# Optimization experiments

Hardware: AMD Instinct MI355X
Metric: run time of the kernel (lower is better)

The kernel has to match this reference:

```python
import jax, jax.numpy as jnp
import numpy as np

N = 100000       # nodes
E = 1600000      # edges
F_IN = 128       # num_node_features
H = 256          # graph_hidden_channels
NHID = 512
NOUT = 256
G = 256          # graphs in batch


def setup_inputs() -> dict:
    key = jax.random.key(0)
    ks = jax.random.split(key, 14)
    x = jax.random.normal(ks[0], (N, F_IN), jnp.float32)
    src = jax.random.randint(ks[1], (E,), 0, N, jnp.int32)
    dst = jax.random.randint(ks[2], (E,), 0, N, jnp.int32)
    batch = jnp.sort(jax.random.randint(ks[3], (N,), 0, G, jnp.int32))
    def lin(k, fan_in, fan_out):
        return jax.random.normal(k, (fan_in, fan_out), jnp.float32) * (1.0 / np.sqrt(fan_in))
    return {
        "x": x, "src": src, "dst": dst, "batch": batch,
        "W1": lin(ks[4], F_IN, H), "b1": jnp.zeros((H,), jnp.float32),
        "W2": lin(ks[5], H, H),    "b2": jnp.zeros((H,), jnp.float32),
        "W3": lin(ks[6], H, H),    "b3": jnp.zeros((H,), jnp.float32),
        "Wm1": lin(ks[7], H, NHID), "bm1": jnp.zeros((NHID,), jnp.float32),
        "Wm2": lin(ks[8], NHID, NOUT), "bm2": jnp.zeros((NOUT,), jnp.float32),
    }


def _gcn_layer(h_in, W, b, src, dst, dinv):
    # GCNConv: transform, then symmetric-normalized aggregation with self-loops.
    h = h_in @ W                                            # [N, out]
    norm = (dinv[src] * dinv[dst])[:, None]                 # [E, 1]
    agg = jax.ops.segment_sum(h[src] * norm, dst, num_segments=N)
    agg = agg + h * (dinv * dinv)[:, None]                  # self-loop term (norm = 1/deg)
    return agg + b


def reference(x, src, dst, batch, W1, b1, W2, b2, W3, b3, Wm1, bm1, Wm2, bm2):
    # degrees include the added self-loop (+1)
    deg = 1.0 + jax.ops.segment_sum(jnp.ones((E,), x.dtype), dst, num_segments=N)
    dinv = jax.lax.rsqrt(deg)                               # deg^{-1/2}

    h = jax.nn.relu(_gcn_layer(x, W1, b1, src, dst, dinv))
    h = jax.nn.relu(_gcn_layer(h, W2, b2, src, dst, dinv))
    h = _gcn_layer(h, W3, b3, src, dst, dinv)               # no relu before pooling

    # global mean pool over graphs
    counts = jax.ops.segment_sum(jnp.ones((N,), x.dtype), batch, num_segments=G)
    pooled = jax.ops.segment_sum(h, batch, num_segments=G) / jnp.maximum(counts, 1.0)[:, None]

    out = jax.nn.relu(pooled @ Wm1 + bm1) @ Wm2 + bm2       # [G, NOUT]
    return out
```

## Files before the change

### kernel.cpp

```cpp
#include <hip/hip_runtime.h>
#include <hip/hip_bf16.h>

#define N_NODES 100000
#define N_EDGES 1600000
#define F_IN    128
#define H       256
#define NHID    512
#define NOUT    256
#define G_GR    256

typedef unsigned short u16;
typedef __attribute__((ext_vector_type(8))) short s16x8;
typedef __attribute__((ext_vector_type(8))) unsigned short u16x8;
typedef __attribute__((ext_vector_type(4))) float f32x4;

__device__ __forceinline__ float bf2f(u16 u) {
    union { unsigned int i; float f; } v; v.i = ((unsigned int)u) << 16; return v.f;
}
__device__ __forceinline__ u16 f2bf(float f) {
    union { float f; unsigned int i; } v; v.f = f;
    unsigned int x = v.i;
    x += 0x7fffu + ((x >> 16) & 1u);
    return (u16)(x >> 16);
}

#define CD_BLKS   1563
#define SPX_BLKS  ((N_NODES * F_IN) / 1024)
#define T1_BLKS   ((F_IN * H) / 256)
#define T2_BLKS   ((H * H) / 256)
#define T3_BLKS   ((H * H) / 256)
#define TM1_BLKS  ((H * NHID) / 256)
#define TM2_BLKS  ((NHID * NOUT) / 256)
#define HEAD_BLKS (CD_BLKS + T1_BLKS + T2_BLKS + T3_BLKS + TM1_BLKS + TM2_BLKS + 2)

__device__ __forceinline__ void transpose_split_body(const float* __restrict__ W,
        u16* __restrict__ thi, u16* __restrict__ tlo, int K, int N, int id) {
    int n = id / K, k = id - n * K;
    float f = W[(size_t)k * N + n];
    u16 h = f2bf(f);
    thi[id] = h;
    tlo[id] = f2bf(f - bf2f(h));
}

__global__ __launch_bounds__(256) void prep_head(
        const int* __restrict__ dst, int* __restrict__ degc,
        const float* __restrict__ W1, u16* __restrict__ t1h, u16* __restrict__ t1l,
        const float* __restrict__ W2, u16* __restrict__ t2h, u16* __restrict__ t2l,
        const float* __restrict__ W3, u16* __restrict__ t3h, u16* __restrict__ t3l,
        const float* __restrict__ Wm1, u16* __restrict__ tm1h, u16* __restrict__ tm1l,
        const float* __restrict__ Wm2, u16* __restrict__ tm2h, u16* __restrict__ tm2l,
        const int* __restrict__ batch, int* __restrict__ goff) {
    int bid = blockIdx.x;
    if (bid < CD_BLKS) {
        int base = bid * 1024 + threadIdx.x;
#pragma unroll
        for (int q = 0; q < 4; q++) {
            int e = base + q * 256;
            if (e < N_EDGES) atomicAdd(&degc[dst[e]], 1);
        }
        return;
    }
    bid -= CD_BLKS;
    if (bid < T1_BLKS) {
        transpose_split_body(W1, t1h, t1l, F_IN, H, bid * 256 + threadIdx.x);
        return;
    }
    bid -= T1_BLKS;
    if (bid < T2_BLKS) {
        transpose_split_body(W2, t2h, t2l, H, H, bid * 256 + threadIdx.x);
        return;
    }
    bid -= T2_BLKS;
    if (bid < T3_BLKS) {
        transpose_split_body(W3, t3h, t3l, H, H, bid * 256 + threadIdx.x);
        return;
    }
    bid -= T3_BLKS;
    if (bid < TM1_BLKS) {
        transpose_split_body(Wm1, tm1h, tm1l, H, NHID, bid * 256 + threadIdx.x);
        return;
    }
    bid -= TM1_BLKS;
    if (bid < TM2_BLKS) {
        transpose_split_body(Wm2, tm2h, tm2l, NHID, NOUT, bid * 256 + threadIdx.x);
        return;
    }
    bid -= TM2_BLKS;
    {
        int g = bid * 256 + threadIdx.x;
        if (g > G_GR) return;
        int lo = 0, hi = N_NODES;
        while (lo < hi) {
            int mid = (lo + hi) >> 1;
            if (batch[mid] < g) lo = mid + 1; else hi = mid;
        }
        goff[g] = lo;
    }
}

__global__ void scan_partial(const int* __restrict__ cnt, int* __restrict__ partial) {
    __shared__ int s[256];
    int t = threadIdx.x;
    int i = blockIdx.x * 256 + t;
    int v = (i < N_NODES) ? cnt[i] : 0;
    s[t] = v; __syncthreads();
    for (int off = 128; off > 0; off >>= 1) {
        if (t < off) s[t] += s[t + off];
        __syncthreads();
    }
    if (t == 0) partial[blockIdx.x] = s[0];
}

__global__ void scan_offsets(int* __restrict__ partial, int nb, int* __restrict__ rowp) {
    __shared__ int s[512];
    int t = threadIdx.x;
    int orig = (t < nb) ? partial[t] : 0;
    s[t] = orig; __syncthreads();
    for (int off = 1; off < 512; off <<= 1) {
        int u = (t >= off) ? s[t - off] : 0;
        __syncthreads();
        s[t] += u;
        __syncthreads();
    }
    if (t < nb) partial[t] = s[t] - orig;
    if (t == 0) rowp[N_NODES] = N_EDGES;
}

__global__ void scan_final_dinv(const int* __restrict__ cnt, const int* __restrict__ partial,
                                int* __restrict__ rowp, int* __restrict__ cur,
                                float* __restrict__ dinv) {
    __shared__ int s[256];
    int t = threadIdx.x;
    int i = blockIdx.x * 256 + t;
    int v = (i < N_NODES) ? cnt[i] : 0;
    s[t] = v; __syncthreads();
    for (int off = 1; off < 256; off <<= 1) {
        int u = (t >= off) ? s[t - off] : 0;
        __syncthreads();
        s[t] += u;
        __syncthreads();
    }
    if (i < N_NODES) {
        int r = partial[blockIdx.x] + s[t] - v;
        rowp[i] = r;
        cur[i] = r;
        dinv[i] = rsqrtf(1.0f + (float)v);
    }
}

__global__ __launch_bounds__(256) void scatter_splitx(
        const int* __restrict__ src, const int* __restrict__ dst,
        const float* __restrict__ dinv, int* __restrict__ cur,
        int2* __restrict__ ep,
        const float* __restrict__ x, u16* __restrict__ x_bf) {
    int bid = blockIdx.x;
    if (bid < CD_BLKS) {
        int base = bid * 1024 + threadIdx.x;
#pragma unroll
        for (int q = 0; q < 4; q++) {
            int e = base + q * 256;
            if (e < N_EDGES) {
                int d = dst[e];
                int s = src[e];
                float w = dinv[d] * dinv[s];
                int pos = atomicAdd(&cur[d], 1);
                int2 v; v.x = s; v.y = __float_as_int(w);
                ep[pos] = v;
            }
        }
        return;
    }
    bid -= CD_BLKS;
    {
        int idx = bid * 256 + threadIdx.x;
        float4 f = *(const float4*)&x[(size_t)idx * 4];
        ushort4 o;
        o.x = f2bf(f.x); o.y = f2bf(f.y); o.z = f2bf(f.z); o.w = f2bf(f.w);
        *(ushort4*)&x_bf[(size_t)idx * 4] = o;
    }
}

__global__ __launch_bounds__(256) void gcn_agg256(
        const u16* __restrict__ in, const int* __restrict__ rowp,
        const int2* __restrict__ ep, const float* __restrict__ dinv,
        u16* __restrict__ outp) {
    int node = blockIdx.x * 8 + (threadIdx.x >> 5);
    int l = threadIdx.x & 31;
    int beg = rowp[node], end = rowp[node + 1];
    float a[8] = {};
    int e = beg;
    int2 pr[8];
    bool have = (e + 8 <= end);
    if (have) {
#pragma unroll
        for (int q = 0; q < 8; q++) pr[q] = ep[e + q];
    }
    while (have) {
        int2 g8[8];
#pragma unroll
        for (int q = 0; q < 8; q++) g8[q] = pr[q];
        int en = e + 8;
        bool haven = (en + 8 <= end);
        if (haven) {
#pragma unroll
            for (int q = 0; q < 8; q++) pr[q] = ep[en + q];
        }
#pragma unroll
        for (int q = 0; q < 8; q++) {
            u16x8 u = *(const u16x8*)&in[(size_t)g8[q].x * H + l * 8];
            float wt = __int_as_float(g8[q].y);
#pragma unroll
            for (int r = 0; r < 8; r++) a[r] += bf2f(u[r]) * wt;
        }
        e = en; have = haven;
    }
    for (; e < end; e++) {
        int2 pe = ep[e];
        float wt = __int_as_float(pe.y);
        u16x8 u = *(const u16x8*)&in[(size_t)pe.x * H + l * 8];
#pragma unroll
        for (int r = 0; r < 8; r++) a[r] += bf2f(u[r]) * wt;
    }
    float di = dinv[node];
    u16x8 us = *(const u16x8*)&in[(size_t)node * H + l * 8];
    float dd = di * di;
    u16x8 o;
#pragma unroll
    for (int r = 0; r < 8; r++) o[r] = f2bf(a[r] + bf2f(us[r]) * dd);
    *(u16x8*)&outp[(size_t)node * H + l * 8] = o;
}

__global__ __launch_bounds__(256) void gcn_agg128(
        const u16* __restrict__ in, const int* __restrict__ rowp,
        const int2* __restrict__ ep, const float* __restrict__ dinv,
        u16* __restrict__ outp) {
    int node = blockIdx.x * 16 + (threadIdx.x >> 4);
    int l = threadIdx.x & 15;
    int beg = rowp[node], end = rowp[node + 1];
    float a[8] = {};
    int e = beg;
    int2 pr[8];
    bool have = (e + 8 <= end);
    if (have) {
#pragma unroll
        for (int q = 0; q < 8; q++) pr[q] = ep[e + q];
    }
    while (have) {
        int2 g8[8];
#pragma unroll
        for (int q = 0; q < 8; q++) g8[q] = pr[q];
        int en = e + 8;
        bool haven = (en + 8 <= end);
        if (haven) {
#pragma unroll
            for (int q = 0; q < 8; q++) pr[q] = ep[en + q];
        }
#pragma unroll
        for (int q = 0; q < 8; q++) {
            u16x8 u = *(const u16x8*)&in[(size_t)g8[q].x * F_IN + l * 8];
            float wt = __int_as_float(g8[q].y);
#pragma unroll
            for (int r = 0; r < 8; r++) a[r] += bf2f(u[r]) * wt;
        }
        e = en; have = haven;
    }
    for (; e < end; e++) {
        int2 pe = ep[e];
        float wt = __int_as_float(pe.y);
        u16x8 u = *(const u16x8*)&in[(size_t)pe.x * F_IN + l * 8];
#pragma unroll
        for (int r = 0; r < 8; r++) a[r] += bf2f(u[r]) * wt;
    }
    float di = dinv[node];
    u16x8 us = *(const u16x8*)&in[(size_t)node * F_IN + l * 8];
    float dd = di * di;
    u16x8 o;
#pragma unroll
    for (int r = 0; r < 8; r++) o[r] = f2bf(a[r] + bf2f(us[r]) * dd);
    *(u16x8*)&outp[(size_t)node * F_IN + l * 8] = o;
}

__global__ __launch_bounds__(256) void gcn_agg_pool(
        const u16* __restrict__ in, const int* __restrict__ rowp,
        const int2* __restrict__ ep, const float* __restrict__ dinv,
        const int* __restrict__ batch, float* __restrict__ poolacc) {
    __shared__ __align__(16) float pacc[8][H];
    __shared__ int gslot[8];
    const int tid = threadIdx.x;
    const int hw = tid >> 5;
    const int l = tid & 31;
    const int node = blockIdx.x * 8 + hw;
    const int gbase = batch[blockIdx.x * 8];

    int beg = rowp[node], end = rowp[node + 1];
    float a[8] = {};
    int e = beg;
    int2 pr[8];
    bool have = (e + 8 <= end);
    if (have) {
#pragma unroll
        for (int q = 0; q < 8; q++) pr[q] = ep[e + q];
    }
    while (have) {
        int2 g8[8];
#pragma unroll
        for (int q = 0; q < 8; q++) g8[q] = pr[q];
        int en = e + 8;
        bool haven = (en + 8 <= end);
        if (haven) {
#pragma unroll
            for (int q = 0; q < 8; q++) pr[q] = ep[en + q];
        }
#pragma unroll
        for (int q = 0; q < 8; q++) {
            u16x8 u = *(const u16x8*)&in[(size_t)g8[q].x * H + l * 8];
            float wt = __int_as_float(g8[q].y);
#pragma unroll
            for (int r = 0; r < 8; r++) a[r] += bf2f(u[r]) * wt;
        }
        e = en; have = haven;
    }
    for (; e < end; e++) {
        int2 pe = ep[e];
        float wt = __int_as_float(pe.y);
        u16x8 u = *(const u16x8*)&in[(size_t)pe.x * H + l * 8];
#pragma unroll
        for (int r = 0; r < 8; r++) a[r] += bf2f(u[r]) * wt;
    }
    float di = dinv[node];
    u16x8 us = *(const u16x8*)&in[(size_t)node * H + l * 8];
    float dd = di * di;
    f32x4 lo4, hi4;
#pragma unroll
    for (int r = 0; r < 4; r++) lo4[r] = a[r] + bf2f(us[r]) * dd;
#pragma unroll
    for (int r = 0; r < 4; r++) hi4[r] = a[r + 4] + bf2f(us[r + 4]) * dd;
    *(f32x4*)&pacc[hw][l * 8] = lo4;
    *(f32x4*)&pacc[hw][l * 8 + 4] = hi4;
    if (l == 0) gslot[hw] = batch[node] - gbase;
    __syncthreads();

    int smax = gslot[7];
    float v[8];
#pragma unroll
    for (int q = 0; q < 8; q++) v[q] = pacc[q][tid];
    for (int s = 0; s <= smax; s++) {
        float acc = 0.f;
#pragma unroll
        for (int q = 0; q < 8; q++)
            if (gslot[q] == s) acc += v[q];
        atomicAdd(&poolacc[(size_t)(gbase + s) * H + tid], acc);
    }
}

__global__ __launch_bounds__(256) void pool_finalize2(
        const float* __restrict__ poolacc, const int* __restrict__ goff,
        u16* __restrict__ phi, u16* __restrict__ plo) {
    int g = blockIdx.x, t = threadIdx.x;
    float c = (float)(goff[g + 1] - goff[g]);
    float acc = poolacc[(size_t)g * H + t] / fmaxf(c, 1.f);
    u16 hv = f2bf(acc);
    phi[g * H + t] = hv;
    plo[g * H + t] = f2bf(acc - bf2f(hv));
}

template<int K, bool RELU>
__global__ __launch_bounds__(256) void gemm_bias(
        const u16* __restrict__ A,
        const u16* __restrict__ Bhi, const u16* __restrict__ Blo,
        const float* __restrict__ bias, u16* __restrict__ C, int M) {
    __shared__ __align__(16) u16 sA[128 * 40];
    __shared__ __align__(16) u16 sB[2 * 128 * 40];
    const int tid = threadIdx.x;
    const int w = tid >> 6, l = tid & 63;
    const int wm = (w & 1) * 64, wn = (w >> 1) * 64;
    const int bm = blockIdx.x * 128, bn = blockIdx.y * 128;
    const int srow = tid >> 2;
    const int schunk = (tid & 3) * 8;
    const int lr = l & 15, lg = (l >> 4) * 8;

    f32x4 acc[4][4] = {};

    for (int k0 = 0; k0 < K; k0 += 32) {
        {
            int r0 = bm + srow, r1 = bm + srow + 64;
            u16x8 v0 = {}, v1 = {};
            if (r0 < M) v0 = *(const u16x8*)&A[(size_t)r0 * K + k0 + schunk];
            if (r1 < M) v1 = *(const u16x8*)&A[(size_t)r1 * K + k0 + schunk];
            *(u16x8*)&sA[srow * 40 + schunk] = v0;
            *(u16x8*)&sA[(srow + 64) * 40 + schunk] = v1;
        }
        {
            int n0 = bn + srow, n1 = bn + srow + 64;
            *(u16x8*)&sB[srow * 40 + schunk] = *(const u16x8*)&Bhi[(size_t)n0 * K + k0 + schunk];
            *(u16x8*)&sB[(srow + 64) * 40 + schunk] = *(const u16x8*)&Bhi[(size_t)n1 * K + k0 + schunk];
            *(u16x8*)&sB[128 * 40 + srow * 40 + schunk] = *(const u16x8*)&Blo[(size_t)n0 * K + k0 + schunk];
            *(u16x8*)&sB[128 * 40 + (srow + 64) * 40 + schunk] = *(const u16x8*)&Blo[(size_t)n1 * K + k0 + schunk];
        }
        __syncthreads();

        s16x8 af[4], bh[4], bl[4];
#pragma unroll
        for (int i = 0; i < 4; i++)
            af[i] = __builtin_bit_cast(s16x8, *(const u16x8*)&sA[(wm + i * 16 + lr) * 40 + lg]);
#pragma unroll
        for (int j = 0; j < 4; j++) {
            bh[j] = __builtin_bit_cast(s16x8, *(const u16x8*)&sB[(wn + j * 16 + lr) * 40 + lg]);
            bl[j] = __builtin_bit_cast(s16x8, *(const u16x8*)&sB[128 * 40 + (wn + j * 16 + lr) * 40 + lg]);
        }
#pragma unroll
        for (int i = 0; i < 4; i++) {
#pragma unroll
            for (int j = 0; j < 4; j++) {
                acc[i][j] = __builtin_amdgcn_mfma_f32_16x16x32_bf16(af[i], bh[j], acc[i][j], 0, 0, 0);
                acc[i][j] = __builtin_amdgcn_mfma_f32_16x16x32_bf16(af[i], bl[j], acc[i][j], 0, 0, 0);
            }
        }
        __syncthreads();
    }

    float bcol[4];
#pragma unroll
    for (int j = 0; j < 4; j++) bcol[j] = bias[bn + wn + j * 16 + lr];

    const int lq = (l >> 4) * 4;
#pragma unroll
    for (int i = 0; i < 4; i++) {
#pragma unroll
        for (int r0 = 0; r0 < 4; r0++) {
            int row = bm + wm + i * 16 + lq + r0;
            if (row < M) {
#pragma unroll
                for (int j = 0; j < 4; j++) {
                    float v = acc[i][j][r0] + bcol[j];
                    if (RELU) v = fmaxf(v, 0.f);
                    C[(size_t)row * H + bn + wn + j * 16 + lr] = f2bf(v);
                }
            }
        }
    }
}

template<int K, int NW, bool RELU, bool F32OUT>
__global__ __launch_bounds__(256) void gemm_split(
        const u16* __restrict__ Ahi, const u16* __restrict__ Alo,
        const u16* __restrict__ Bhi, const u16* __restrict__ Blo,
        const float* __restrict__ bias,
        u16* __restrict__ Chi, u16* __restrict__ Clo, float* __restrict__ Cf,
        int M) {
    __shared__ __align__(16) u16 sA[2 * 128 * 40];
    __shared__ __align__(16) u16 sB[2 * 128 * 40];
    const int tid = threadIdx.x;
    const int w = tid >> 6, l = tid & 63;
    const int wm = (w & 1) * 64, wn = (w >> 1) * 64;
    const int bm = blockIdx.x * 128, bn = blockIdx.y * 128;
    const int srow = tid >> 2;
    const int schunk = (tid & 3) * 8;
    const int lr = l & 15, lg = (l >> 4) * 8;

    f32x4 acc[4][4] = {};

    for (int k0 = 0; k0 < K; k0 += 32) {
        {
            int r0 = bm + srow, r1 = bm + srow + 64;
            u16x8 v0 = {}, v1 = {}, w0 = {}, w1 = {};
            if (r0 < M) {
                v0 = *(const u16x8*)&Ahi[(size_t)r0 * K + k0 + schunk];
                w0 = *(const u16x8*)&Alo[(size_t)r0 * K + k0 + schunk];
            }
            if (r1 < M) {
                v1 = *(const u16x8*)&Ahi[(size_t)r1 * K + k0 + schunk];
                w1 = *(const u16x8*)&Alo[(size_t)r1 * K + k0 + schunk];
            }
            *(u16x8*)&sA[srow * 40 + schunk] = v0;
            *(u16x8*)&sA[(srow + 64) * 40 + schunk] = v1;
            *(u16x8*)&sA[128 * 40 + srow * 40 + schunk] = w0;
            *(u16x8*)&sA[128 * 40 + (srow + 64) * 40 + schunk] = w1;
        }
        {
            int n0 = bn + srow, n1 = bn + srow + 64;
            *(u16x8*)&sB[srow * 40 + schunk] = *(const u16x8*)&Bhi[(size_t)n0 * K + k0 + schunk];
            *(u16x8*)&sB[(srow + 64) * 40 + schunk] = *(const u16x8*)&Bhi[(size_t)n1 * K + k0 + schunk];
            *(u16x8*)&sB[128 * 40 + srow * 40 + schunk] = *(const u16x8*)&Blo[(size_t)n0 * K + k0 + schunk];
            *(u16x8*)&sB[128 * 40 + (srow + 64) * 40 + schunk] = *(const u16x8*)&Blo[(size_t)n1 * K + k0 + schunk];
        }
        __syncthreads();

        s16x8 af[4], al[4], bh[4], bl[4];
#pragma unroll
        for (int i = 0; i < 4; i++) {
            af[i] = __builtin_bit_cast(s16x8, *(const u16x8*)&sA[(wm + i * 16 + lr) * 40 + lg]);
            al[i] = __builtin_bit_cast(s16x8, *(const u16x8*)&sA[128 * 40 + (wm + i * 16 + lr) * 40 + lg]);
        }
#pragma unroll
        for (int j = 0; j < 4; j++) {
            bh[j] = __builtin_bit_cast(s16x8, *(const u16x8*)&sB[(wn + j * 16 + lr) * 40 + lg]);
            bl[j] = __builtin_bit_cast(s16x8, *(const u16x8*)&sB[128 * 40 + (wn + j * 16 + lr) * 40 + lg]);
        }
#pragma unroll
        for (int i = 0; i < 4; i++) {
#pragma unroll
            for (int j = 0; j < 4; j++) {
                acc[i][j] = __builtin_amdgcn_mfma_f32_16x16x32_bf16(af[i], bh[j], acc[i][j], 0, 0, 0);
                acc[i][j] = __builtin_amdgcn_mfma_f32_16x16x32_bf16(af[i], bl[j], acc[i][j], 0, 0, 0);
                acc[i][j] = __builtin_amdgcn_mfma_f32_16x16x32_bf16(al[i], bh[j], acc[i][j], 0, 0, 0);
            }
        }
        __syncthreads();
    }

    float bcol[4];
#pragma unroll
    for (int j = 0; j < 4; j++) bcol[j] = bias[bn + wn + j * 16 + lr];

    const int lq = (l >> 4) * 4;
#pragma unroll
    for (int i = 0; i < 4; i++) {
#pragma unroll
        for (int r0 = 0; r0 < 4; r0++) {
            int row = bm + wm + i * 16 + lq + r0;
            if (row < M) {
#pragma unroll
                for (int j = 0; j < 4; j++) {
                    float v = acc[i][j][r0] + bcol[j];
                    if (RELU) v = fmaxf(v, 0.f);
                    size_t idx = (size_t)row * NW + bn + wn + j * 16 + lr;
                    if (F32OUT) {
                        Cf[idx] = v;
                    } else {
                        u16 hv = f2bf(v);
                        Chi[idx] = hv;
                        Clo[idx] = f2bf(v - bf2f(hv));
                    }
                }
            }
        }
    }
}

extern "C" void kernel_launch(void* const* d_in, const int* in_sizes, int n_in,
                              void* d_out, int out_size, void* d_ws, size_t ws_size,
                              hipStream_t stream) {
    const float* x   = (const float*)d_in[0];
    const int*   src = (const int*)d_in[1];
    const int*   dst = (const int*)d_in[2];
    const int*   bat = (const int*)d_in[3];
    const float* W1  = (const float*)d_in[4];  const float* b1  = (const float*)d_in[5];
    const float* W2  = (const float*)d_in[6];  const float* b2  = (const float*)d_in[7];
    const float* W3  = (const float*)d_in[8];  const float* b3  = (const float*)d_in[9];
    const float* Wm1 = (const float*)d_in[10]; const float* bm1 = (const float*)d_in[11];
    const float* Wm2 = (const float*)d_in[12]; const float* bm2 = (const float*)d_in[13];
    float* out = (float*)d_out;

    char* p = (char*)d_ws;
    auto carve = [&](size_t bytes) -> void* {
        void* r = (void*)p;
        p += (bytes + 511) & ~(size_t)511;
        return r;
    };
    u16*   x_bf    = (u16*)  carve((size_t)N_NODES * F_IN * 2);
    u16*   aggX    = (u16*)  carve((size_t)N_NODES * F_IN * 2);
    u16*   bufA    = (u16*)  carve((size_t)N_NODES * H * 2);
    u16*   bufB    = (u16*)  carve((size_t)N_NODES * H * 2);
    float* dinv    = (float*)carve((size_t)N_NODES * 4);
    int*   degc    = (int*)  carve((size_t)N_NODES * 4);
    int*   rowp    = (int*)  carve((size_t)(N_NODES + 1) * 4);
    int*   cur     = (int*)  carve((size_t)N_NODES * 4);
    int2*  ep      = (int2*) carve((size_t)N_EDGES * 8);
    int*   partial = (int*)  carve(4096);
    int*   goff    = (int*)  carve((size_t)(G_GR + 1) * 4);
    u16*   Wt1_hi  = (u16*)  carve((size_t)F_IN * H * 2);
    u16*   Wt1_lo  = (u16*)  carve((size_t)F_IN * H * 2);
    u16*   Wt2_hi  = (u16*)  carve((size_t)H * H * 2);
    u16*   Wt2_lo  = (u16*)  carve((size_t)H * H * 2);
    u16*   Wt3_hi  = (u16*)  carve((size_t)H * H * 2);
    u16*   Wt3_lo  = (u16*)  carve((size_t)H * H * 2);
    u16*   Wm1t_hi = (u16*)  carve((size_t)H * NHID * 2);
    u16*   Wm1t_lo = (u16*)  carve((size_t)H * NHID * 2);
    u16*   Wm2t_hi = (u16*)  carve((size_t)NHID * NOUT * 2);
    u16*   Wm2t_lo = (u16*)  carve((size_t)NHID * NOUT * 2);
    u16*   p_hi    = (u16*)  carve((size_t)G_GR * H * 2);
    u16*   p_lo    = (u16*)  carve((size_t)G_GR * H * 2);
    u16*   y_hi    = (u16*)  carve((size_t)G_GR * H * 2);
    u16*   y_lo    = (u16*)  carve((size_t)G_GR * H * 2);
    u16*   hd_hi   = (u16*)  carve((size_t)G_GR * NHID * 2);
    u16*   hd_lo   = (u16*)  carve((size_t)G_GR * NHID * 2);
    float* poolacc = (float*)carve((size_t)G_GR * H * 4);

    const int NB = (N_NODES + 255) / 256;

    hipMemsetAsync(degc, 0, (size_t)N_NODES * 4, stream);
    hipMemsetAsync(poolacc, 0, (size_t)G_GR * H * 4, stream);
    prep_head<<<HEAD_BLKS, 256, 0, stream>>>(dst, degc,
                                             W1, Wt1_hi, Wt1_lo,
                                             W2, Wt2_hi, Wt2_lo,
                                             W3, Wt3_hi, Wt3_lo,
                                             Wm1, Wm1t_hi, Wm1t_lo,
                                             Wm2, Wm2t_hi, Wm2t_lo, bat, goff);
    scan_partial<<<NB, 256, 0, stream>>>(degc, partial);
    scan_offsets<<<1, 512, 0, stream>>>(partial, NB, rowp);
    scan_final_dinv<<<NB, 256, 0, stream>>>(degc, partial, rowp, cur, dinv);
    scatter_splitx<<<CD_BLKS + SPX_BLKS, 256, 0, stream>>>(src, dst, dinv, cur, ep, x, x_bf);

    dim3 ggrid((N_NODES + 127) / 128, 2);

    gcn_agg128<<<N_NODES / 16, 256, 0, stream>>>(x_bf, rowp, ep, dinv, aggX);
    gemm_bias<F_IN, true><<<ggrid, 256, 0, stream>>>(aggX, Wt1_hi, Wt1_lo, b1, bufA, N_NODES);
    gcn_agg256<<<N_NODES / 8, 256, 0, stream>>>(bufA, rowp, ep, dinv, bufB);
    gemm_bias<H, true><<<ggrid, 256, 0, stream>>>(bufB, Wt2_hi, Wt2_lo, b2, bufA, N_NODES);
    gcn_agg_pool<<<N_NODES / 8, 256, 0, stream>>>(bufA, rowp, ep, dinv, bat, poolacc);
    pool_finalize2<<<G_GR, 256, 0, stream>>>(poolacc, goff, p_hi, p_lo);

    dim3 g3(2, 2), gm1(2, 4), gm2(2, 2);
    gemm_split<H, H, false, false><<<g3, 256, 0, stream>>>(
        p_hi, p_lo, Wt3_hi, Wt3_lo, b3, y_hi, y_lo, nullptr, G_GR);
    gemm_split<H, NHID, true, false><<<gm1, 256, 0, stream>>>(
        y_hi, y_lo, Wm1t_hi, Wm1t_lo, bm1, hd_hi, hd_lo, nullptr, G_GR);
    gemm_split<NHID, NOUT, false, true><<<gm2, 256, 0, stream>>>(
        hd_hi, hd_lo, Wm2t_hi, Wm2t_lo, bm2, nullptr, nullptr, out, G_GR);
}
```

Measured before the change: 724.4 us.

## Pack source index and degree into 4-byte edge entries; tile weight transposes

Edge records shrink from 8-byte (src, weight) pairs to a 4-byte word holding the source index in the low 17 bits and the source degree above them. Each aggregation kernel rebuilds the edge weight on the fly as dinv[node]*rsqrt(1+deg_src). This halves edge-list traffic in the scatter and in all three aggregation passes, at the cost of one rsqrt per edge per lane. Weight transpose/split also moves to 64x64 shared-memory tiles so reads and writes are coalesced. The packing assumes node count under 2^17 and degree under 2^15.

```diff
diff --git a/kernel.cpp b/kernel.cpp
--- a/kernel.cpp
+++ b/kernel.cpp
@@ -10,9 +10,13 @@
 #define G_GR    256
 
 typedef unsigned short u16;
+typedef unsigned int u32;
 typedef __attribute__((ext_vector_type(8))) short s16x8;
 typedef __attribute__((ext_vector_type(8))) unsigned short u16x8;
 typedef __attribute__((ext_vector_type(4))) float f32x4;
+
+#define SRC_MASK 0x1FFFFu
+#define DEG_SHIFT 17
 
 __device__ __forceinline__ float bf2f(u16 u) {
     union { unsigned int i; float f; } v; v.i = ((unsigned int)u) << 16; return v.f;
@@ -26,20 +30,32 @@
 
 #define CD_BLKS   1563
 #define SPX_BLKS  ((N_NODES * F_IN) / 1024)
-#define T1_BLKS   ((F_IN * H) / 256)
-#define T2_BLKS   ((H * H) / 256)
-#define T3_BLKS   ((H * H) / 256)
-#define TM1_BLKS  ((H * NHID) / 256)
-#define TM2_BLKS  ((NHID * NOUT) / 256)
-#define HEAD_BLKS (CD_BLKS + T1_BLKS + T2_BLKS + T3_BLKS + TM1_BLKS + TM2_BLKS + 2)
-
-__device__ __forceinline__ void transpose_split_body(const float* __restrict__ W,
-        u16* __restrict__ thi, u16* __restrict__ tlo, int K, int N, int id) {
-    int n = id / K, k = id - n * K;
-    float f = W[(size_t)k * N + n];
-    u16 h = f2bf(f);
-    thi[id] = h;
-    tlo[id] = f2bf(f - bf2f(h));
+#define T1_TILES  ((F_IN / 64) * (H / 64))
+#define T2_TILES  ((H / 64) * (H / 64))
+#define T3_TILES  ((H / 64) * (H / 64))
+#define TM1_TILES ((H / 64) * (NHID / 64))
+#define TM2_TILES ((NHID / 64) * (NOUT / 64))
+#define HEAD_BLKS (CD_BLKS + T1_TILES + T2_TILES + T3_TILES + TM1_TILES + TM2_TILES + 2)
+
+__device__ __forceinline__ void transpose_tile(float (*tile)[65],
+        const float* __restrict__ W, u16* __restrict__ thi, u16* __restrict__ tlo,
+        int K, int N, int tileIdx) {
+    const int ntn = N >> 6;
+    const int tk = tileIdx / ntn, tn = tileIdx - tk * ntn;
+    const int t = threadIdx.x;
+    const int c = t & 63, r4 = t >> 6;
+#pragma unroll
+    for (int i = 0; i < 64; i += 4)
+        tile[r4 + i][c] = W[(size_t)(tk * 64 + r4 + i) * N + tn * 64 + c];
+    __syncthreads();
+#pragma unroll
+    for (int i = 0; i < 64; i += 4) {
+        int n = tn * 64 + r4 + i, k = tk * 64 + c;
+        float f = tile[c][r4 + i];
+        u16 h = f2bf(f);
+        thi[(size_t)n * K + k] = h;
+        tlo[(size_t)n * K + k] = f2bf(f - bf2f(h));
+    }
 }
 
 __global__ __launch_bounds__(256) void prep_head(
@@ -50,6 +66,7 @@
         const float* __restrict__ Wm1, u16* __restrict__ tm1h, u16* __restrict__ tm1l,
         const float* __restrict__ Wm2, u16* __restrict__ tm2h, u16* __restrict__ tm2l,
         const int* __restrict__ batch, int* __restrict__ goff) {
+    __shared__ float tile[64][65];
     int bid = blockIdx.x;
     if (bid < CD_BLKS) {
         int base = bid * 1024 + threadIdx.x;
@@ -61,31 +78,16 @@
         return;
     }
     bid -= CD_BLKS;
-    if (bid < T1_BLKS) {
-        transpose_split_body(W1, t1h, t1l, F_IN, H, bid * 256 + threadIdx.x);
-        return;
-    }
-    bid -= T1_BLKS;
-    if (bid < T2_BLKS) {
-        transpose_split_body(W2, t2h, t2l, H, H, bid * 256 + threadIdx.x);
-        return;
-    }
-    bid -= T2_BLKS;
-    if (bid < T3_BLKS) {
-        transpose_split_body(W3, t3h, t3l, H, H, bid * 256 + threadIdx.x);
-        return;
-    }
-    bid -= T3_BLKS;
-    if (bid < TM1_BLKS) {
-        transpose_split_body(Wm1, tm1h, tm1l, H, NHID, bid * 256 + threadIdx.x);
-        return;
-    }
-    bid -= TM1_BLKS;
-    if (bid < TM2_BLKS) {
-        transpose_split_body(Wm2, tm2h, tm2l, NHID, NOUT, bid * 256 + threadIdx.x);
-        return;
-    }
-    bid -= TM2_BLKS;
+    if (bid < T1_TILES) { transpose_tile(tile, W1, t1h, t1l, F_IN, H, bid); return; }
+    bid -= T1_TILES;
+    if (bid < T2_TILES) { transpose_tile(tile, W2, t2h, t2l, H, H, bid); return; }
+    bid -= T2_TILES;
+    if (bid < T3_TILES) { transpose_tile(tile, W3, t3h, t3l, H, H, bid); return; }
+    bid -= T3_TILES;
+    if (bid < TM1_TILES) { transpose_tile(tile, Wm1, tm1h, tm1l, H, NHID, bid); return; }
+    bid -= TM1_TILES;
+    if (bid < TM2_TILES) { transpose_tile(tile, Wm2, tm2h, tm2l, NHID, NOUT, bid); return; }
+    bid -= TM2_TILES;
     {
         int g = bid * 256 + threadIdx.x;
         if (g > G_GR) return;
@@ -128,7 +130,7 @@
 
 __global__ void scan_final_dinv(const int* __restrict__ cnt, const int* __restrict__ partial,
                                 int* __restrict__ rowp, int* __restrict__ cur,
-                                float* __restrict__ dinv) {
+                                float* __restrict__ dinv, u32* __restrict__ pack) {
     __shared__ int s[256];
     int t = threadIdx.x;
     int i = blockIdx.x * 256 + t;
@@ -145,13 +147,14 @@
         rowp[i] = r;
         cur[i] = r;
         dinv[i] = rsqrtf(1.0f + (float)v);
+        pack[i] = (u32)i | ((u32)v << DEG_SHIFT);
     }
 }
 
 __global__ __launch_bounds__(256) void scatter_splitx(
         const int* __restrict__ src, const int* __restrict__ dst,
-        const float* __restrict__ dinv, int* __restrict__ cur,
-        int2* __restrict__ ep,
+        const u32* __restrict__ pack, int* __restrict__ cur,
+        u32* __restrict__ ep4,
         const float* __restrict__ x, u16* __restrict__ x_bf) {
     int bid = blockIdx.x;
     if (bid < CD_BLKS) {
@@ -162,10 +165,9 @@
             if (e < N_EDGES) {
                 int d = dst[e];
                 int s = src[e];
-                float w = dinv[d] * dinv[s];
+                u32 pk = pack[s];
                 int pos = atomicAdd(&cur[d], 1);
-                int2 v; v.x = s; v.y = __float_as_int(w);
-                ep[pos] = v;
+                ep4[pos] = pk;
             }
         }
         return;
@@ -182,48 +184,48 @@
 
 __global__ __launch_bounds__(256) void gcn_agg256(
         const u16* __restrict__ in, const int* __restrict__ rowp,
-        const int2* __restrict__ ep, const float* __restrict__ dinv,
+        const u32* __restrict__ ep4, const float* __restrict__ dinv,
         u16* __restrict__ outp) {
     int node = blockIdx.x * 8 + (threadIdx.x >> 5);
     int l = threadIdx.x & 31;
     int beg = rowp[node], end = rowp[node + 1];
+    float dnode = dinv[node];
     float a[8] = {};
     int e = beg;
-    int2 pr[8];
+    u32 pr[8];
     bool have = (e + 8 <= end);
     if (have) {
 #pragma unroll
-        for (int q = 0; q < 8; q++) pr[q] = ep[e + q];
+        for (int q = 0; q < 8; q++) pr[q] = ep4[e + q];
     }
     while (have) {
-        int2 g8[8];
+        u32 g8[8];
 #pragma unroll
         for (int q = 0; q < 8; q++) g8[q] = pr[q];
         int en = e + 8;
         bool haven = (en + 8 <= end);
         if (haven) {
 #pragma unroll
-            for (int q = 0; q < 8; q++) pr[q] = ep[en + q];
+            for (int q = 0; q < 8; q++) pr[q] = ep4[en + q];
         }
 #pragma unroll
         for (int q = 0; q < 8; q++) {
-            u16x8 u = *(const u16x8*)&in[(size_t)g8[q].x * H + l * 8];
-            float wt = __int_as_float(g8[q].y);
+            u16x8 u = *(const u16x8*)&in[(size_t)(g8[q] & SRC_MASK) * H + l * 8];
+            float wt = dnode * rsqrtf(1.0f + (float)(g8[q] >> DEG_SHIFT));
 #pragma unroll
             for (int r = 0; r < 8; r++) a[r] += bf2f(u[r]) * wt;
         }
         e = en; have = haven;
     }
     for (; e < end; e++) {
-        int2 pe = ep[e];
-        float wt = __int_as_float(pe.y);
-        u16x8 u = *(const u16x8*)&in[(size_t)pe.x * H + l * 8];
+        u32 pe = ep4[e];
+        float wt = dnode * rsqrtf(1.0f + (float)(pe >> DEG_SHIFT));
+        u16x8 u = *(const u16x8*)&in[(size_t)(pe & SRC_MASK) * H + l * 8];
 #pragma unroll
         for (int r = 0; r < 8; r++) a[r] += bf2f(u[r]) * wt;
     }
-    float di = dinv[node];
     u16x8 us = *(const u16x8*)&in[(size_t)node * H + l * 8];
-    float dd = di * di;
+    float dd = dnode * dnode;
     u16x8 o;
 #pragma unroll
     for (int r = 0; r < 8; r++) o[r] = f2bf(a[r] + bf2f(us[r]) * dd);
@@ -232,48 +234,48 @@
 
 __global__ __launch_bounds__(256) void gcn_agg128(
         const u16* __restrict__ in, const int* __restrict__ rowp,
-        const int2* __restrict__ ep, const float* __restrict__ dinv,
+        const u32* __restrict__ ep4, const float* __restrict__ dinv,
         u16* __restrict__ outp) {
     int node = blockIdx.x * 16 + (threadIdx.x >> 4);
     int l = threadIdx.x & 15;
     int beg = rowp[node], end = rowp[node + 1];
+    float dnode = dinv[node];
     float a[8] = {};
     int e = beg;
-    int2 pr[8];
+    u32 pr[8];
     bool have = (e + 8 <= end);
     if (have) {
 #pragma unroll
-        for (int q = 0; q < 8; q++) pr[q] = ep[e + q];
+        for (int q = 0; q < 8; q++) pr[q] = ep4[e + q];
     }
     while (have) {
-        int2 g8[8];
+        u32 g8[8];
 #pragma unroll
         for (int q = 0; q < 8; q++) g8[q] = pr[q];
         int en = e + 8;
         bool haven = (en + 8 <= end);
         if (haven) {
 #pragma unroll
-            for (int q = 0; q < 8; q++) pr[q] = ep[en + q];
+            for (int q = 0; q < 8; q++) pr[q] = ep4[en + q];
         }
 #pragma unroll
         for (int q = 0; q < 8; q++) {
-            u16x8 u = *(const u16x8*)&in[(size_t)g8[q].x * F_IN + l * 8];
-            float wt = __int_as_float(g8[q].y);
+            u16x8 u = *(const u16x8*)&in[(size_t)(g8[q] & SRC_MASK) * F_IN + l * 8];
+            float wt = dnode * rsqrtf(1.0f + (float)(g8[q] >> DEG_SHIFT));
 #pragma unroll
             for (int r = 0; r < 8; r++) a[r] += bf2f(u[r]) * wt;
         }
         e = en; have = haven;
     }
     for (; e < end; e++) {
-        int2 pe = ep[e];
-        float wt = __int_as_float(pe.y);
-        u16x8 u = *(const u16x8*)&in[(size_t)pe.x * F_IN + l * 8];
+        u32 pe = ep4[e];
+        float wt = dnode * rsqrtf(1.0f + (float)(pe >> DEG_SHIFT));
+        u16x8 u = *(const u16x8*)&in[(size_t)(pe & SRC_MASK) * F_IN + l * 8];
 #pragma unroll
         for (int r = 0; r < 8; r++) a[r] += bf2f(u[r]) * wt;
     }
-    float di = dinv[node];
     u16x8 us = *(const u16x8*)&in[(size_t)node * F_IN + l * 8];
-    float dd = di * di;
+    float dd = dnode * dnode;
     u16x8 o;
 #pragma unroll
     for (int r = 0; r < 8; r++) o[r] = f2bf(a[r] + bf2f(us[r]) * dd);
@@ -282,7 +284,7 @@
 
 __global__ __launch_bounds__(256) void gcn_agg_pool(
         const u16* __restrict__ in, const int* __restrict__ rowp,
-        const int2* __restrict__ ep, const float* __restrict__ dinv,
+        const u32* __restrict__ ep4, const float* __restrict__ dinv,
         const int* __restrict__ batch, float* __restrict__ poolacc) {
     __shared__ __align__(16) float pacc[8][H];
     __shared__ int gslot[8];
@@ -293,43 +295,43 @@
     const int gbase = batch[blockIdx.x * 8];
 
     int beg = rowp[node], end = rowp[node + 1];
+    float dnode = dinv[node];
     float a[8] = {};
     int e = beg;
-    int2 pr[8];
+    u32 pr[8];
     bool have = (e + 8 <= end);
     if (have) {
 #pragma unroll
-        for (int q = 0; q < 8; q++) pr[q] = ep[e + q];
+        for (int q = 0; q < 8; q++) pr[q] = ep4[e + q];
     }
     while (have) {
-        int2 g8[8];
+        u32 g8[8];
 #pragma unroll
         for (int q = 0; q < 8; q++) g8[q] = pr[q];
         int en = e + 8;
         bool haven = (en + 8 <= end);
         if (haven) {
 #pragma unroll
-            for (int q = 0; q < 8; q++) pr[q] = ep[en + q];
+            for (int q = 0; q < 8; q++) pr[q] = ep4[en + q];
         }
 #pragma unroll
         for (int q = 0; q < 8; q++) {
-            u16x8 u = *(const u16x8*)&in[(size_t)g8[q].x * H + l * 8];
-            float wt = __int_as_float(g8[q].y);
+            u16x8 u = *(const u16x8*)&in[(size_t)(g8[q] & SRC_MASK) * H + l * 8];
+            float wt = dnode * rsqrtf(1.0f + (float)(g8[q] >> DEG_SHIFT));
 #pragma unroll
             for (int r = 0; r < 8; r++) a[r] += bf2f(u[r]) * wt;
         }
         e = en; have = haven;
     }
     for (; e < end; e++) {
-        int2 pe = ep[e];
-        float wt = __int_as_float(pe.y);
-        u16x8 u = *(const u16x8*)&in[(size_t)pe.x * H + l * 8];
+        u32 pe = ep4[e];
+        float wt = dnode * rsqrtf(1.0f + (float)(pe >> DEG_SHIFT));
+        u16x8 u = *(const u16x8*)&in[(size_t)(pe & SRC_MASK) * H + l * 8];
 #pragma unroll
         for (int r = 0; r < 8; r++) a[r] += bf2f(u[r]) * wt;
     }
-    float di = dinv[node];
     u16x8 us = *(const u16x8*)&in[(size_t)node * H + l * 8];
-    float dd = di * di;
+    float dd = dnode * dnode;
     f32x4 lo4, hi4;
 #pragma unroll
     for (int r = 0; r < 4; r++) lo4[r] = a[r] + bf2f(us[r]) * dd;
@@ -566,7 +568,8 @@
     int*   degc    = (int*)  carve((size_t)N_NODES * 4);
     int*   rowp    = (int*)  carve((size_t)(N_NODES + 1) * 4);
     int*   cur     = (int*)  carve((size_t)N_NODES * 4);
-    int2*  ep      = (int2*) carve((size_t)N_EDGES * 8);
+    u32*   ep4     = (u32*)  carve((size_t)N_EDGES * 4);
+    u32*   pack    = (u32*)  carve((size_t)N_NODES * 4);
     int*   partial = (int*)  carve(4096);
     int*   goff    = (int*)  carve((size_t)(G_GR + 1) * 4);
     u16*   Wt1_hi  = (u16*)  carve((size_t)F_IN * H * 2);
@@ -599,16 +602,16 @@
                                              Wm2, Wm2t_hi, Wm2t_lo, bat, goff);
     scan_partial<<<NB, 256, 0, stream>>>(degc, partial);
     scan_offsets<<<1, 512, 0, stream>>>(partial, NB, rowp);
-    scan_final_dinv<<<NB, 256, 0, stream>>>(degc, partial, rowp, cur, dinv);
-    scatter_splitx<<<CD_BLKS + SPX_BLKS, 256, 0, stream>>>(src, dst, dinv, cur, ep, x, x_bf);
+    scan_final_dinv<<<NB, 256, 0, stream>>>(degc, partial, rowp, cur, dinv, pack);
+    scatter_splitx<<<CD_BLKS + SPX_BLKS, 256, 0, stream>>>(src, dst, pack, cur, ep4, x, x_bf);
 
     dim3 ggrid((N_NODES + 127) / 128, 2);
 
-    gcn_agg128<<<N_NODES / 16, 256, 0, stream>>>(x_bf, rowp, ep, dinv, aggX);
+    gcn_agg128<<<N_NODES / 16, 256, 0, stream>>>(x_bf, rowp, ep4, dinv, aggX);
     gemm_bias<F_IN, true><<<ggrid, 256, 0, stream>>>(aggX, Wt1_hi, Wt1_lo, b1, bufA, N_NODES);
-    gcn_agg256<<<N_NODES / 8, 256, 0, stream>>>(bufA, rowp, ep, dinv, bufB);
+    gcn_agg256<<<N_NODES / 8, 256, 0, stream>>>(bufA, rowp, ep4, dinv, bufB);
     gemm_bias<H, true><<<ggrid, 256, 0, stream>>>(bufB, Wt2_hi, Wt2_lo, b2, bufA, N_NODES);
-    gcn_agg_pool<<<N_NODES / 8, 256, 0, stream>>>(bufA, rowp, ep, dinv, bat, poolacc);
+    gcn_agg_pool<<<N_NODES / 8, 256, 0, stream>>>(bufA, rowp, ep4, dinv, bat, poolacc);
     pool_finalize2<<<G_GR, 256, 0, stream>>>(poolacc, goff, p_hi, p_lo);
 
     dim3 g3(2, 2), gm1(2, 4), gm2(2, 2);
```

Measured after the change: 693.8 us. -4.2%, faster.
